# Performance work log

Measured on AMD Instinct MI355X. Metric: run time of the kernel, lower is better.

## Reference

```python
import jax, jax.numpy as jnp
import numpy as np

N, F_IN, HID, EMB, HEADS, E = 20000, 256, 256, 128, 8, 160000
NEG_SLOPE = 0.2


def setup_inputs() -> dict:
    key = jax.random.key(0)
    ks = jax.random.split(key, 16)
    s = lambda fan: 1.0 / np.sqrt(fan)
    inp = {
        "x": jax.random.normal(ks[0], (N, F_IN), jnp.float32),
        "edge_index": jax.random.randint(ks[1], (2, E), 0, N, jnp.int64),
        "W1": jax.random.normal(ks[2], (F_IN, HID), jnp.float32) * s(F_IN),
        "b1": jnp.zeros((HID,), jnp.float32),
        "W2": jax.random.normal(ks[3], (HID, HID), jnp.float32) * s(HID),
        "b2": jnp.zeros((HID,), jnp.float32),
        "W3": jax.random.normal(ks[4], (HID, EMB), jnp.float32) * s(HID),
        "b3": jnp.zeros((EMB,), jnp.float32),
        "Wg": jax.random.normal(ks[5], (EMB, HEADS * EMB), jnp.float32) * s(EMB),
        "att_src": jax.random.normal(ks[6], (HEADS, EMB), jnp.float32) * s(EMB),
        "att_dst": jax.random.normal(ks[7], (HEADS, EMB), jnp.float32) * s(EMB),
        "bg": jnp.zeros((HEADS * EMB,), jnp.float32),
        "Wh1": jax.random.normal(ks[8], (HEADS * EMB, HID), jnp.float32) * s(HEADS * EMB),
        "bh1": jnp.zeros((HID,), jnp.float32),
        "Wh2": jax.random.normal(ks[9], (HID, 1), jnp.float32) * s(HID),
        "bh2": jnp.zeros((1,), jnp.float32),
    }
    return inp


def _gcn(x, W, b, src, dst, dinv):
    h = x @ W                                   # [N, out]
    msg = h[src] * (dinv[src] * dinv[dst])[:, None]  # gather + edge scale
    return jax.ops.segment_sum(msg, dst, N) + b


def _gat(x, Wg, att_src, att_dst, bg, src, dst):
    h = (x @ Wg).reshape(N, HEADS, EMB)          # [N, H, C]
    a_s = jnp.einsum('nhc,hc->nh', h, att_src)   # [N, H]
    a_d = jnp.einsum('nhc,hc->nh', h, att_dst)
    e = jax.nn.leaky_relu(a_s[src] + a_d[dst], NEG_SLOPE)  # [Etot, H]
    m = jax.ops.segment_max(e, dst, N)           # per-dst softmax max
    ex = jnp.exp(e - m[dst])
    denom = jax.ops.segment_sum(ex, dst, N)
    alpha = ex / denom[dst]                      # [Etot, H]
    out = jax.ops.segment_sum(h[src] * alpha[:, :, None], dst, N)
    return out.reshape(N, HEADS * EMB) + bg


def reference(x, edge_index, W1, b1, W2, b2, W3, b3, Wg, att_src, att_dst, bg, Wh1, bh1, Wh2, bh2):
    loops = jnp.arange(N, dtype=edge_index.dtype)
    src = jnp.concatenate([edge_index[0], loops])
    dst = jnp.concatenate([edge_index[1], loops])
    deg = jax.ops.segment_sum(jnp.ones_like(dst, dtype=x.dtype), dst, N)
    dinv = jax.lax.rsqrt(jnp.maximum(deg, 1.0))  # deg >= 1 due to self-loops

    h = jax.nn.relu(_gcn(x, W1, b1, src, dst, dinv))
    h = jax.nn.relu(_gcn(h, W2, b2, src, dst, dinv))
    h = jax.nn.relu(_gcn(h, W3, b3, src, dst, dinv))
    h = _gat(h, Wg, att_src, att_dst, bg, src, dst)
    z = jax.nn.relu(h @ Wh1 + bh1)
    logits = (z @ Wh2 + bh2).squeeze(-1)         # [N]
    w = jax.nn.sigmoid(logits)
    return jax.nn.softmax(w, axis=0)
```

## Files before the change

kernel.cpp:

```cpp
#include <hip/hip_runtime.h>
#include <math.h>

#define NN 20000
#define HEADS 8
#define GDIM 1024
#define M_PAD 20096

typedef _Float16 f16;
typedef f16 f16x2  __attribute__((ext_vector_type(2)));
typedef f16 f16x4v __attribute__((ext_vector_type(4)));
typedef f16 f16x8v __attribute__((ext_vector_type(8)));
typedef float f32x4 __attribute__((ext_vector_type(4)));

__device__ __forceinline__ float lrelu(float x){ return x > 0.f ? x : 0.2f*x; }

__global__ __launch_bounds__(256) void init_k(int* __restrict__ zbase, int zn,
        const float* __restrict__ W1, const float* __restrict__ W2, const float* __restrict__ W3,
        const float* __restrict__ Wg, const float* __restrict__ Wh1,
        f16* __restrict__ wt1, f16* __restrict__ wt2, f16* __restrict__ wt3,
        f16* __restrict__ wtg, f16* __restrict__ wth1)
{
    int t = blockIdx.x*256 + threadIdx.x;
    if (t < zn){ zbase[t] = 0; return; }
    t -= zn;
    if (t < 65536){ int k = t >> 8, n = t & 255; wt1[n*256 + k] = (f16)W1[t]; return; }
    t -= 65536;
    if (t < 65536){ int k = t >> 8, n = t & 255; wt2[n*256 + k] = (f16)W2[t]; return; }
    t -= 65536;
    if (t < 32768){ int k = t >> 7, n = t & 127; wt3[n*256 + k] = (f16)W3[t]; return; }
    t -= 32768;
    if (t < 131072){ int k = t >> 10, n = t & 1023; wtg[n*128 + k] = (f16)Wg[t]; return; }
    t -= 131072;
    if (t < 262144){ int k = t >> 8, n = t & 255; wth1[n*1024 + k] = (f16)Wh1[t]; return; }
}

__global__ __launch_bounds__(256) void hist_k(const int* __restrict__ dst, int* __restrict__ cnt, int E){
    int i = blockIdx.x*256 + threadIdx.x;
    if (i < E) atomicAdd(&cnt[dst[i]], 1);
}
__global__ __launch_bounds__(1024) void scan_k(const int* __restrict__ cnt, int* __restrict__ row_off,
                                               float* __restrict__ dinv){
    __shared__ int tot[1024];
    int t = threadIdx.x;
    const int CH = 20;
    int base = t*CH;
    int loc[CH]; int s = 0;
    #pragma unroll
    for (int i = 0; i < CH; ++i){
        int v = (base+i < NN) ? cnt[base+i] : 0;
        loc[i] = s; s += v;
    }
    tot[t] = s; __syncthreads();
    for (int off = 1; off < 1024; off <<= 1){
        int v = (t >= off) ? tot[t-off] : 0;
        __syncthreads();
        tot[t] += v;
        __syncthreads();
    }
    int pre = (t == 0) ? 0 : tot[t-1];
    #pragma unroll
    for (int i = 0; i < CH; ++i)
        if (base+i < NN){
            row_off[base+i] = pre + loc[i];
            dinv[base+i] = rsqrtf((float)cnt[base+i] + 1.f);
        }
    if (t == 1023) row_off[NN] = tot[1023];
}
__global__ __launch_bounds__(256) void scatter_k(const int* __restrict__ src, const int* __restrict__ dst,
        const int* __restrict__ row_off, int* __restrict__ cursor, int* __restrict__ src_sorted, int E){
    int i = blockIdx.x*256 + threadIdx.x;
    if (i >= E) return;
    int d = dst[i];
    int pos = row_off[d] + atomicAdd(&cursor[d], 1);
    src_sorted[pos] = src[i];
}

template<int EPI, int BN, bool A_F32, bool RELU, bool HAS_BIAS>
__global__ __launch_bounds__(256,2) void gemm_f16_k(
        const void* __restrict__ Av, const f16* __restrict__ Bt,
        const float* __restrict__ bias, void* __restrict__ C,
        const float* __restrict__ att_s, const float* __restrict__ att_d,
        float* __restrict__ as_out, float* __restrict__ ad_out,
        const float* __restrict__ Wh2, float* __restrict__ logit,
        int M, int N, int K)
{
    constexpr int WN = BN/2;
    constexpr int NJ = WN/16;
    __shared__ __align__(16) f16 As[128*32];
    __shared__ __align__(16) f16 Bs[BN*32];
    __shared__ float sred[2][128][2];
    const int tid  = threadIdx.x;
    const int lane = tid & 63;
    const int wave = tid >> 6;
    const int wm = (wave >> 1) * 64, wn = (wave & 1) * WN;
    const int l15 = lane & 15, quad = lane >> 4;
    const int m0 = blockIdx.y * 128, n0 = blockIdx.x * BN;

    const int r1 = tid >> 2;
    const int ce = (tid & 3) * 8;
    const int rowA0 = m0 + r1, rowA1 = rowA0 + 64;
    const f16*  Ah = (const f16*)Av;
    const float* Af = (const float*)Av;
    const f16* B0 = Bt + (size_t)(n0 + r1) * K + ce;
    const f16* B1 = B0 + (size_t)64 * K;

    f32x4 acc[4][NJ] = {};
    for (int k0 = 0; k0 < K; k0 += 32){
        if (A_F32){
            f16x8v h0 = {}, h1 = {};
            if (rowA0 < M){
                float4 p = *(const float4*)(Af + (size_t)rowA0*K + k0 + ce);
                float4 q = *(const float4*)(Af + (size_t)rowA0*K + k0 + ce + 4);
                h0[0]=(f16)p.x; h0[1]=(f16)p.y; h0[2]=(f16)p.z; h0[3]=(f16)p.w;
                h0[4]=(f16)q.x; h0[5]=(f16)q.y; h0[6]=(f16)q.z; h0[7]=(f16)q.w;
            }
            if (rowA1 < M){
                float4 p = *(const float4*)(Af + (size_t)rowA1*K + k0 + ce);
                float4 q = *(const float4*)(Af + (size_t)rowA1*K + k0 + ce + 4);
                h1[0]=(f16)p.x; h1[1]=(f16)p.y; h1[2]=(f16)p.z; h1[3]=(f16)p.w;
                h1[4]=(f16)q.x; h1[5]=(f16)q.y; h1[6]=(f16)q.z; h1[7]=(f16)q.w;
            }
            *(f16x8v*)&As[tid*8]        = h0;
            *(f16x8v*)&As[tid*8 + 2048] = h1;
        } else {
            *(uint4*)&As[tid*8]        = *(const uint4*)(Ah + (size_t)rowA0*K + k0 + ce);
            *(uint4*)&As[tid*8 + 2048] = *(const uint4*)(Ah + (size_t)rowA1*K + k0 + ce);
        }
        *(uint4*)&Bs[tid*8] = *(const uint4*)(B0 + k0);
        if (BN == 128)
            *(uint4*)&Bs[tid*8 + 2048] = *(const uint4*)(B1 + k0);
        __syncthreads();
        f16x8v af[4], bf[NJ];
        #pragma unroll
        for (int i = 0; i < 4; ++i)
            af[i] = *(const f16x8v*)&As[(wm + i*16 + l15)*32 + quad*8];
        #pragma unroll
        for (int j = 0; j < NJ; ++j)
            bf[j] = *(const f16x8v*)&Bs[(wn + j*16 + l15)*32 + quad*8];
        #pragma unroll
        for (int i = 0; i < 4; ++i)
            #pragma unroll
            for (int j = 0; j < NJ; ++j)
                acc[i][j] = __builtin_amdgcn_mfma_f32_16x16x32_f16(af[i], bf[j], acc[i][j], 0, 0, 0);
        __syncthreads();
    }

    if (EPI == 2){
        float b4[NJ], w4[NJ];
        #pragma unroll
        for (int j = 0; j < NJ; ++j){
            int cg = n0 + wn + j*16 + l15;
            b4[j] = bias[cg]; w4[j] = Wh2[cg];
        }
        #pragma unroll
        for (int i = 0; i < 4; ++i)
            #pragma unroll
            for (int r = 0; r < 4; ++r){
                float ps = 0.f;
                #pragma unroll
                for (int j = 0; j < NJ; ++j){
                    float v = fmaxf(acc[i][j][r] + b4[j], 0.f);
                    ps = fmaf(v, w4[j], ps);
                }
                ps += __shfl_xor(ps, 1, 64); ps += __shfl_xor(ps, 2, 64);
                ps += __shfl_xor(ps, 4, 64); ps += __shfl_xor(ps, 8, 64);
                if (l15 == 0){
                    int row = m0 + wm + i*16 + quad*4 + r;
                    if (row < M) unsafeAtomicAdd(&logit[row], ps);
                }
            }
        return;
    }

    #pragma unroll
    for (int i = 0; i < 4; ++i){
        int rb = m0 + wm + i*16 + quad*4;
        #pragma unroll
        for (int j = 0; j < NJ; ++j){
            int col = n0 + wn + j*16 + l15;
            float bv = HAS_BIAS ? bias[col] : 0.f;
            #pragma unroll
            for (int r = 0; r < 4; ++r){
                int row = rb + r;
                if (row >= M) continue;
                float v = acc[i][j][r] + bv;
                if (RELU) v = fmaxf(v, 0.f);
                ((f16*)C)[(size_t)row*N + col] = (f16)v;
            }
        }
    }

    if (EPI == 1){
        const int h = blockIdx.x;
        float ats[NJ], atd[NJ];
        #pragma unroll
        for (int j = 0; j < NJ; ++j){
            int c = wn + j*16 + l15;
            ats[j] = att_s[h*128 + c]; atd[j] = att_d[h*128 + c];
        }
        #pragma unroll
        for (int i = 0; i < 4; ++i)
            #pragma unroll
            for (int r = 0; r < 4; ++r){
                float ps = 0.f, pd = 0.f;
                #pragma unroll
                for (int j = 0; j < NJ; ++j){
                    float a = acc[i][j][r];
                    ps = fmaf(a, ats[j], ps); pd = fmaf(a, atd[j], pd);
                }
                ps += __shfl_xor(ps, 1, 64); ps += __shfl_xor(ps, 2, 64);
                ps += __shfl_xor(ps, 4, 64); ps += __shfl_xor(ps, 8, 64);
                pd += __shfl_xor(pd, 1, 64); pd += __shfl_xor(pd, 2, 64);
                pd += __shfl_xor(pd, 4, 64); pd += __shfl_xor(pd, 8, 64);
                if (l15 == 0){
                    int rl = wm + i*16 + quad*4 + r;
                    sred[0][rl][wn >> 6] = ps;
                    sred[1][rl][wn >> 6] = pd;
                }
            }
        __syncthreads();
        if (tid < 128){
            int row = m0 + tid;
            if (row < M){
                as_out[row*HEADS + h] = sred[0][tid][0] + sred[0][tid][1];
                ad_out[row*HEADS + h] = sred[1][tid][0] + sred[1][tid][1];
            }
        }
    }
}

template<int F>
__global__ __launch_bounds__(256) void gcn_agg_f16_k(const f16* __restrict__ h, const int* __restrict__ row_off,
        const int* __restrict__ srcs, const float* __restrict__ dinv, const float* __restrict__ bias,
        f16* __restrict__ out)
{
    int wv = (blockIdx.x*256 + threadIdx.x) >> 6;
    int lane = threadIdx.x & 63;
    if (wv >= NN) return;
    float di = dinv[wv];
    int p = row_off[wv], r1 = row_off[wv+1];
    if (F == 256){
        f16x4v v = *(const f16x4v*)(h + (size_t)wv*256 + lane*4);
        float c = di*di;
        float a0 = (float)v[0]*c, a1 = (float)v[1]*c, a2 = (float)v[2]*c, a3 = (float)v[3]*c;
        for (; p+4 <= r1; p += 4){
            int s0 = srcs[p], s1 = srcs[p+1], s2 = srcs[p+2], s3 = srcs[p+3];
            float c0 = dinv[s0]*di, c1 = dinv[s1]*di, c2 = dinv[s2]*di, c3 = dinv[s3]*di;
            f16x4v u0 = *(const f16x4v*)(h + (size_t)s0*256 + lane*4);
            f16x4v u1 = *(const f16x4v*)(h + (size_t)s1*256 + lane*4);
            f16x4v u2 = *(const f16x4v*)(h + (size_t)s2*256 + lane*4);
            f16x4v u3 = *(const f16x4v*)(h + (size_t)s3*256 + lane*4);
            a0 = fmaf((float)u3[0], c3, fmaf((float)u2[0], c2, fmaf((float)u1[0], c1, fmaf((float)u0[0], c0, a0))));
            a1 = fmaf((float)u3[1], c3, fmaf((float)u2[1], c2, fmaf((float)u1[1], c1, fmaf((float)u0[1], c0, a1))));
            a2 = fmaf((float)u3[2], c3, fmaf((float)u2[2], c2, fmaf((float)u1[2], c1, fmaf((float)u0[2], c0, a2))));
            a3 = fmaf((float)u3[3], c3, fmaf((float)u2[3], c2, fmaf((float)u1[3], c1, fmaf((float)u0[3], c0, a3))));
        }
        for (; p < r1; ++p){
            int s0 = srcs[p];
            float c0 = dinv[s0]*di;
            f16x4v u0 = *(const f16x4v*)(h + (size_t)s0*256 + lane*4);
            a0 = fmaf((float)u0[0], c0, a0); a1 = fmaf((float)u0[1], c0, a1);
            a2 = fmaf((float)u0[2], c0, a2); a3 = fmaf((float)u0[3], c0, a3);
        }
        float4 bv = *(const float4*)(bias + lane*4);
        f16x4v o;
        o[0] = (f16)fmaxf(a0 + bv.x, 0.f); o[1] = (f16)fmaxf(a1 + bv.y, 0.f);
        o[2] = (f16)fmaxf(a2 + bv.z, 0.f); o[3] = (f16)fmaxf(a3 + bv.w, 0.f);
        *(f16x4v*)(out + (size_t)wv*256 + lane*4) = o;
    } else {
        f16x2 v = *(const f16x2*)(h + (size_t)wv*128 + lane*2);
        float c = di*di;
        float a0 = (float)v[0]*c, a1 = (float)v[1]*c;
        for (; p+4 <= r1; p += 4){
            int s0 = srcs[p], s1 = srcs[p+1], s2 = srcs[p+2], s3 = srcs[p+3];
            float c0 = dinv[s0]*di, c1 = dinv[s1]*di, c2 = dinv[s2]*di, c3 = dinv[s3]*di;
            f16x2 u0 = *(const f16x2*)(h + (size_t)s0*128 + lane*2);
            f16x2 u1 = *(const f16x2*)(h + (size_t)s1*128 + lane*2);
            f16x2 u2 = *(const f16x2*)(h + (size_t)s2*128 + lane*2);
            f16x2 u3 = *(const f16x2*)(h + (size_t)s3*128 + lane*2);
            a0 = fmaf((float)u3[0], c3, fmaf((float)u2[0], c2, fmaf((float)u1[0], c1, fmaf((float)u0[0], c0, a0))));
            a1 = fmaf((float)u3[1], c3, fmaf((float)u2[1], c2, fmaf((float)u1[1], c1, fmaf((float)u0[1], c0, a1))));
        }
        for (; p < r1; ++p){
            int s0 = srcs[p];
            float c0 = dinv[s0]*di;
            f16x2 u0 = *(const f16x2*)(h + (size_t)s0*128 + lane*2);
            a0 = fmaf((float)u0[0], c0, a0); a1 = fmaf((float)u0[1], c0, a1);
        }
        float2 bv = *(const float2*)(bias + lane*2);
        f16x2 o;
        o[0] = (f16)fmaxf(a0 + bv.x, 0.f); o[1] = (f16)fmaxf(a1 + bv.y, 0.f);
        *(f16x2*)(out + (size_t)wv*128 + lane*2) = o;
    }
}

__global__ __launch_bounds__(256) void gat_soft_k(const int* __restrict__ row_off, const int* __restrict__ srcs,
        const float* __restrict__ a_s, const float* __restrict__ a_d,
        float* __restrict__ ex_sorted, float* __restrict__ alpha_self, float* __restrict__ inv_den)
{
    int t = blockIdx.x*256 + threadIdx.x;
    if (t >= NN*HEADS) return;
    int d = t >> 3, h = t & 7;
    float ad = a_d[t];
    float eself = lrelu(a_s[t] + ad);
    float m = eself;
    int r0 = row_off[d], r1 = row_off[d+1];
    for (int p = r0; p < r1; ++p){
        int s = srcs[p];
        m = fmaxf(m, lrelu(a_s[s*HEADS + h] + ad));
    }
    float den = expf(eself - m);
    for (int p = r0; p < r1; ++p){
        int s = srcs[p];
        float x = expf(lrelu(a_s[s*HEADS + h] + ad) - m);
        ex_sorted[(size_t)p*HEADS + h] = x;
        den += x;
    }
    float id = 1.f / den;
    alpha_self[t] = expf(eself - m) * id;
    inv_den[t]    = id;
}
__global__ __launch_bounds__(256) void gat_out_f16_k(const f16* __restrict__ hg, const int* __restrict__ row_off,
        const int* __restrict__ srcs, const float* __restrict__ exs, const float* __restrict__ aself,
        const float* __restrict__ idn, const float* __restrict__ bg, f16* __restrict__ gat)
{
    int gw = (blockIdx.x*256 + threadIdx.x) >> 6;
    int lane = threadIdx.x & 63;
    int node = gw >> 1;
    if (node >= NN) return;
    int colbase = (gw & 1)*512 + lane*8;
    int hh = colbase >> 7;
    int nh = node*HEADS + hh;
    float as = aself[nh];
    float id = idn[nh];
    const f16* table = hg + colbase;
    f16x8v v = *(const f16x8v*)(table + (size_t)node*GDIM);
    float acc[8];
    #pragma unroll
    for (int q = 0; q < 8; ++q) acc[q] = (float)v[q]*as;
    int p = row_off[node], r1 = row_off[node+1];
    for (; p+4 <= r1; p += 4){
        int s0 = srcs[p], s1 = srcs[p+1], s2 = srcs[p+2], s3 = srcs[p+3];
        float al0 = exs[(size_t)p*HEADS + hh] * id;
        float al1 = exs[(size_t)(p+1)*HEADS + hh] * id;
        float al2 = exs[(size_t)(p+2)*HEADS + hh] * id;
        float al3 = exs[(size_t)(p+3)*HEADS + hh] * id;
        f16x8v u0 = *(const f16x8v*)(table + (size_t)s0*GDIM);
        f16x8v u1 = *(const f16x8v*)(table + (size_t)s1*GDIM);
        f16x8v u2 = *(const f16x8v*)(table + (size_t)s2*GDIM);
        f16x8v u3 = *(const f16x8v*)(table + (size_t)s3*GDIM);
        #pragma unroll
        for (int q = 0; q < 8; ++q)
            acc[q] = fmaf((float)u3[q], al3, fmaf((float)u2[q], al2,
                     fmaf((float)u1[q], al1, fmaf((float)u0[q], al0, acc[q]))));
    }
    for (; p < r1; ++p){
        int s0 = srcs[p];
        float al0 = exs[(size_t)p*HEADS + hh] * id;
        f16x8v u0 = *(const f16x8v*)(table + (size_t)s0*GDIM);
        #pragma unroll
        for (int q = 0; q < 8; ++q) acc[q] = fmaf((float)u0[q], al0, acc[q]);
    }
    float4 b0 = *(const float4*)(bg + colbase);
    float4 b1 = *(const float4*)(bg + colbase + 4);
    f16x8v o;
    o[0]=(f16)(acc[0]+b0.x); o[1]=(f16)(acc[1]+b0.y); o[2]=(f16)(acc[2]+b0.z); o[3]=(f16)(acc[3]+b0.w);
    o[4]=(f16)(acc[4]+b1.x); o[5]=(f16)(acc[5]+b1.y); o[6]=(f16)(acc[6]+b1.z); o[7]=(f16)(acc[7]+b1.w);
    *(f16x8v*)(gat + (size_t)node*GDIM + colbase) = o;
}

__global__ __launch_bounds__(256) void head_sum_k(const float* __restrict__ logit, const float* __restrict__ bh2,
                                                  float* __restrict__ w, float* __restrict__ red){
    __shared__ float sm[256];
    int i = blockIdx.x*256 + threadIdx.x;
    float v = 0.f;
    if (i < NN){
        float s = 1.f / (1.f + expf(-(logit[i] + bh2[0])));
        w[i] = s;
        v = expf(s);
    }
    sm[threadIdx.x] = v; __syncthreads();
    for (int off = 128; off; off >>= 1){
        if (threadIdx.x < off) sm[threadIdx.x] += sm[threadIdx.x+off];
        __syncthreads();
    }
    if (!threadIdx.x) unsafeAtomicAdd(&red[0], sm[0]);
}
__global__ __launch_bounds__(256) void final_k(const float* __restrict__ w, const float* __restrict__ red,
                                               float* __restrict__ out){
    int i = blockIdx.x*256 + threadIdx.x;
    if (i >= NN) return;
    out[i] = expf(w[i]) / red[0];
}

extern "C" void kernel_launch(void* const* d_in, const int* in_sizes, int n_in,
                              void* d_out, int out_size, void* d_ws, size_t ws_size,
                              hipStream_t stream) {
    const float* x   = (const float*)d_in[0];
    const int*   ei  = (const int*)  d_in[1];
    const float* W1  = (const float*)d_in[2];
    const float* b1  = (const float*)d_in[3];
    const float* W2  = (const float*)d_in[4];
    const float* b2  = (const float*)d_in[5];
    const float* W3  = (const float*)d_in[6];
    const float* b3  = (const float*)d_in[7];
    const float* Wg  = (const float*)d_in[8];
    const float* att_src = (const float*)d_in[9];
    const float* att_dst = (const float*)d_in[10];
    const float* bg  = (const float*)d_in[11];
    const float* Wh1 = (const float*)d_in[12];
    const float* bh1 = (const float*)d_in[13];
    const float* Wh2 = (const float*)d_in[14];
    const float* bh2 = (const float*)d_in[15];
    float* out = (float*)d_out;

    const int E = in_sizes[1] / 2;
    const int* src = ei;
    const int* dst = ei + E;

    float* ws = (float*)d_ws;
    size_t o = 0;
    auto alloc = [&](size_t nfloats){ float* p = ws + o; o += (nfloats + 3) & ~(size_t)3; return p; };
    int* cnt    = (int*)alloc(NN);
    int* cursor = (int*)alloc(NN);
    float* logit= alloc(NN);
    float* red  = alloc(8);
    const int ZERO_N = 3*NN + 8;

    f16* wt1   = (f16*)alloc(65536/2);
    f16* wt2   = (f16*)alloc(65536/2);
    f16* wt3   = (f16*)alloc(32768/2);
    f16* wtg   = (f16*)alloc(131072/2);
    f16* wth1  = (f16*)alloc(262144/2);
    f16* fH    = (f16*)alloc((size_t)M_PAD*256/2);
    f16* fG    = (f16*)alloc((size_t)M_PAD*256/2);
    f16* hg    = (f16*)alloc((size_t)M_PAD*GDIM/2);
    f16* gat   = (f16*)alloc((size_t)M_PAD*GDIM/2);
    float* dinv = alloc(NN);
    float* a_s  = alloc((size_t)NN*HEADS);
    float* a_d  = alloc((size_t)NN*HEADS);
    float* aself= alloc((size_t)NN*HEADS);
    float* idn  = alloc((size_t)NN*HEADS);
    float* exs  = alloc((size_t)E*HEADS);
    float* wsig = alloc(NN);
    int* row_off= (int*)alloc(NN+1);
    int* src_srt= (int*)alloc(E);

    const int nb  = (NN + 255)/256;
    const int eb  = (E + 255)/256;
    const int nwb = (NN + 3)/4;
    const dim3 blk(256);
    const int MT = M_PAD/128;

    const int INIT_T = ZERO_N + 65536*2 + 32768 + 131072 + 262144;
    init_k<<<(INIT_T + 255)/256, blk, 0, stream>>>(cnt, ZERO_N, W1, W2, W3, Wg, Wh1,
                                                   wt1, wt2, wt3, wtg, wth1);
    hist_k<<<eb, blk, 0, stream>>>(dst, cnt, E);
    scan_k<<<1, 1024, 0, stream>>>(cnt, row_off, dinv);
    scatter_k<<<eb, blk, 0, stream>>>(src, dst, row_off, cursor, src_srt, E);

    gemm_f16_k<0,64,true,false,false><<<dim3(4, MT), blk, 0, stream>>>(
        x, wt1, nullptr, fH, nullptr, nullptr, nullptr, nullptr, nullptr, nullptr, NN, 256, 256);
    gcn_agg_f16_k<256><<<nwb, blk, 0, stream>>>(fH, row_off, src_srt, dinv, b1, fG);
    gemm_f16_k<0,64,false,false,false><<<dim3(4, MT), blk, 0, stream>>>(
        fG, wt2, nullptr, fH, nullptr, nullptr, nullptr, nullptr, nullptr, nullptr, NN, 256, 256);
    gcn_agg_f16_k<256><<<nwb, blk, 0, stream>>>(fH, row_off, src_srt, dinv, b2, fG);
    gemm_f16_k<0,64,false,false,false><<<dim3(2, MT), blk, 0, stream>>>(
        fG, wt3, nullptr, fH, nullptr, nullptr, nullptr, nullptr, nullptr, nullptr, NN, 128, 256);
    gcn_agg_f16_k<128><<<nwb, blk, 0, stream>>>(fH, row_off, src_srt, dinv, b3, fG);

    gemm_f16_k<1,128,false,false,false><<<dim3(8, MT), blk, 0, stream>>>(
        fG, wtg, nullptr, hg, att_src, att_dst, a_s, a_d, nullptr, nullptr, NN, 1024, 128);
    gat_soft_k<<<(NN*HEADS)/256, blk, 0, stream>>>(row_off, src_srt, a_s, a_d, exs, aself, idn);
    gat_out_f16_k<<<NN/2, blk, 0, stream>>>(hg, row_off, src_srt, exs, aself, idn, bg, gat);

    gemm_f16_k<2,128,false,true,true><<<dim3(2, MT), blk, 0, stream>>>(
        gat, wth1, bh1, nullptr, nullptr, nullptr, nullptr, nullptr, Wh2, logit, NN, 256, 1024);

    head_sum_k<<<nb, blk, 0, stream>>>(logit, bh2, wsig, red);
    final_k<<<nb, blk, 0, stream>>>(wsig, red, out);
}
```

Baseline: 379.6 us.

## Fold GAT projection into attention vectors and head weight, aggregate raw embeddings

Removes the 128→1024 GAT projection GEMM. Attention logits are computed directly from the 128-dim embeddings using precomputed Wg·att vectors. The weighted neighbour aggregation now runs on the 128-dim input, once per head, and the resulting 1024-wide aggregate is multiplied by a fused Wg·Wh1 weight with a folded bias. This avoids writing and gathering the 1024-wide hg table. The cost is a new per-call weight-fusion kernel, and fp16 rounding now applies to the fused weight product instead.

```diff
diff --git a/kernel.cpp b/kernel.cpp
--- a/kernel.cpp
+++ b/kernel.cpp
@@ -3,7 +3,6 @@
 
 #define NN 20000
 #define HEADS 8
-#define GDIM 1024
 #define M_PAD 20096
 
 typedef _Float16 f16;
@@ -16,9 +15,9 @@
 
 __global__ __launch_bounds__(256) void init_k(int* __restrict__ zbase, int zn,
         const float* __restrict__ W1, const float* __restrict__ W2, const float* __restrict__ W3,
-        const float* __restrict__ Wg, const float* __restrict__ Wh1,
+        const float* __restrict__ Wg, const float* __restrict__ att_src, const float* __restrict__ att_dst,
         f16* __restrict__ wt1, f16* __restrict__ wt2, f16* __restrict__ wt3,
-        f16* __restrict__ wtg, f16* __restrict__ wth1)
+        float* __restrict__ was_s, float* __restrict__ was_d)
 {
     int t = blockIdx.x*256 + threadIdx.x;
     if (t < zn){ zbase[t] = 0; return; }
@@ -29,9 +28,53 @@
     t -= 65536;
     if (t < 32768){ int k = t >> 7, n = t & 127; wt3[n*256 + k] = (f16)W3[t]; return; }
     t -= 32768;
-    if (t < 131072){ int k = t >> 10, n = t & 1023; wtg[n*128 + k] = (f16)Wg[t]; return; }
-    t -= 131072;
-    if (t < 262144){ int k = t >> 8, n = t & 255; wth1[n*1024 + k] = (f16)Wh1[t]; return; }
+    if (t < 2048){
+        int which = t >> 10, r = t & 1023, k = r >> 3, h = r & 7;
+        const float* att = which ? att_dst : att_src;
+        float s = 0.f;
+        for (int c = 0; c < 128; ++c)
+            s = fmaf(Wg[k*1024 + h*128 + c], att[h*128 + c], s);
+        (which ? was_d : was_s)[k*8 + h] = s;
+    }
+}
+
+__global__ __launch_bounds__(256) void wc_k(const float* __restrict__ Wg, const float* __restrict__ Wh1,
+        const float* __restrict__ bg, const float* __restrict__ bh1,
+        f16* __restrict__ wc_t, float* __restrict__ biasc)
+{
+    __shared__ float col[1024];
+    __shared__ float red[256];
+    const int j = blockIdx.x, t = threadIdx.x;
+    float bsum = 0.f;
+    #pragma unroll
+    for (int i = 0; i < 4; ++i){
+        int kk = i*256 + t;
+        float v = Wh1[(size_t)kk*256 + j];
+        col[kk] = v;
+        bsum = fmaf(bg[kk], v, bsum);
+    }
+    red[t] = bsum; __syncthreads();
+    for (int off = 128; off; off >>= 1){
+        if (t < off) red[t] += red[t+off];
+        __syncthreads();
+    }
+    if (!t) biasc[j] = red[0] + bh1[j];
+    #pragma unroll
+    for (int i = 0; i < 4; ++i){
+        int k = i*256 + t;
+        int h = k >> 7, kk = k & 127;
+        const float* wg = Wg + (size_t)kk*1024 + h*128;
+        const float* cl = col + h*128;
+        float s = 0.f;
+        for (int c = 0; c < 128; c += 4){
+            float4 wv = *(const float4*)(wg + c);
+            s = fmaf(wv.x, cl[c],   s);
+            s = fmaf(wv.y, cl[c+1], s);
+            s = fmaf(wv.z, cl[c+2], s);
+            s = fmaf(wv.w, cl[c+3], s);
+        }
+        wc_t[(size_t)j*1024 + k] = (f16)s;
+    }
 }
 
 __global__ __launch_bounds__(256) void hist_k(const int* __restrict__ dst, int* __restrict__ cnt, int E){
@@ -79,8 +122,6 @@
 __global__ __launch_bounds__(256,2) void gemm_f16_k(
         const void* __restrict__ Av, const f16* __restrict__ Bt,
         const float* __restrict__ bias, void* __restrict__ C,
-        const float* __restrict__ att_s, const float* __restrict__ att_d,
-        float* __restrict__ as_out, float* __restrict__ ad_out,
         const float* __restrict__ Wh2, float* __restrict__ logit,
         int M, int N, int K)
 {
@@ -88,7 +129,6 @@
     constexpr int NJ = WN/16;
     __shared__ __align__(16) f16 As[128*32];
     __shared__ __align__(16) f16 Bs[BN*32];
-    __shared__ float sred[2][128][2];
     const int tid  = threadIdx.x;
     const int lane = tid & 63;
     const int wave = tid >> 6;
@@ -189,44 +229,6 @@
             }
         }
     }
-
-    if (EPI == 1){
-        const int h = blockIdx.x;
-        float ats[NJ], atd[NJ];
-        #pragma unroll
-        for (int j = 0; j < NJ; ++j){
-            int c = wn + j*16 + l15;
-            ats[j] = att_s[h*128 + c]; atd[j] = att_d[h*128 + c];
-        }
-        #pragma unroll
-        for (int i = 0; i < 4; ++i)
-            #pragma unroll
-            for (int r = 0; r < 4; ++r){
-                float ps = 0.f, pd = 0.f;
-                #pragma unroll
-                for (int j = 0; j < NJ; ++j){
-                    float a = acc[i][j][r];
-                    ps = fmaf(a, ats[j], ps); pd = fmaf(a, atd[j], pd);
-                }
-                ps += __shfl_xor(ps, 1, 64); ps += __shfl_xor(ps, 2, 64);
-                ps += __shfl_xor(ps, 4, 64); ps += __shfl_xor(ps, 8, 64);
-                pd += __shfl_xor(pd, 1, 64); pd += __shfl_xor(pd, 2, 64);
-                pd += __shfl_xor(pd, 4, 64); pd += __shfl_xor(pd, 8, 64);
-                if (l15 == 0){
-                    int rl = wm + i*16 + quad*4 + r;
-                    sred[0][rl][wn >> 6] = ps;
-                    sred[1][rl][wn >> 6] = pd;
-                }
-            }
-        __syncthreads();
-        if (tid < 128){
-            int row = m0 + tid;
-            if (row < M){
-                as_out[row*HEADS + h] = sred[0][tid][0] + sred[0][tid][1];
-                ad_out[row*HEADS + h] = sred[1][tid][0] + sred[1][tid][1];
-            }
-        }
-    }
 }
 
 template<int F>
@@ -294,6 +296,30 @@
     }
 }
 
+__global__ __launch_bounds__(256) void asd_k(const f16* __restrict__ fG,
+        const float* __restrict__ was_s, const float* __restrict__ was_d,
+        float* __restrict__ a_s, float* __restrict__ a_d)
+{
+    int wv = (blockIdx.x*256 + threadIdx.x) >> 6;
+    int lane = threadIdx.x & 63;
+    if (wv >= NN) return;
+    f16x2 v = *(const f16x2*)(fG + (size_t)wv*128 + lane*2);
+    float v0 = (float)v[0], v1 = (float)v[1];
+    const float* ws = was_s + lane*16;
+    const float* wd = was_d + lane*16;
+    #pragma unroll
+    for (int h = 0; h < 8; ++h){
+        float s = fmaf(v1, ws[8+h], v0*ws[h]);
+        float d = fmaf(v1, wd[8+h], v0*wd[h]);
+        #pragma unroll
+        for (int off = 1; off < 64; off <<= 1){
+            s += __shfl_xor(s, off, 64);
+            d += __shfl_xor(d, off, 64);
+        }
+        if (lane == 0){ a_s[wv*8 + h] = s; a_d[wv*8 + h] = d; }
+    }
+}
+
 __global__ __launch_bounds__(256) void gat_soft_k(const int* __restrict__ row_off, const int* __restrict__ srcs,
         const float* __restrict__ a_s, const float* __restrict__ a_d,
         float* __restrict__ ex_sorted, float* __restrict__ alpha_self, float* __restrict__ inv_den)
@@ -320,53 +346,61 @@
     alpha_self[t] = expf(eself - m) * id;
     inv_den[t]    = id;
 }
-__global__ __launch_bounds__(256) void gat_out_f16_k(const f16* __restrict__ hg, const int* __restrict__ row_off,
+
+__global__ __launch_bounds__(256) void agg_k(const f16* __restrict__ fG, const int* __restrict__ row_off,
         const int* __restrict__ srcs, const float* __restrict__ exs, const float* __restrict__ aself,
-        const float* __restrict__ idn, const float* __restrict__ bg, f16* __restrict__ gat)
-{
-    int gw = (blockIdx.x*256 + threadIdx.x) >> 6;
+        const float* __restrict__ idn, f16* __restrict__ agg)
+{
+    int wv = (blockIdx.x*256 + threadIdx.x) >> 6;
     int lane = threadIdx.x & 63;
-    int node = gw >> 1;
-    if (node >= NN) return;
-    int colbase = (gw & 1)*512 + lane*8;
-    int hh = colbase >> 7;
-    int nh = node*HEADS + hh;
-    float as = aself[nh];
-    float id = idn[nh];
-    const f16* table = hg + colbase;
-    f16x8v v = *(const f16x8v*)(table + (size_t)node*GDIM);
-    float acc[8];
-    #pragma unroll
-    for (int q = 0; q < 8; ++q) acc[q] = (float)v[q]*as;
-    int p = row_off[node], r1 = row_off[node+1];
-    for (; p+4 <= r1; p += 4){
-        int s0 = srcs[p], s1 = srcs[p+1], s2 = srcs[p+2], s3 = srcs[p+3];
-        float al0 = exs[(size_t)p*HEADS + hh] * id;
-        float al1 = exs[(size_t)(p+1)*HEADS + hh] * id;
-        float al2 = exs[(size_t)(p+2)*HEADS + hh] * id;
-        float al3 = exs[(size_t)(p+3)*HEADS + hh] * id;
-        f16x8v u0 = *(const f16x8v*)(table + (size_t)s0*GDIM);
-        f16x8v u1 = *(const f16x8v*)(table + (size_t)s1*GDIM);
-        f16x8v u2 = *(const f16x8v*)(table + (size_t)s2*GDIM);
-        f16x8v u3 = *(const f16x8v*)(table + (size_t)s3*GDIM);
-        #pragma unroll
-        for (int q = 0; q < 8; ++q)
-            acc[q] = fmaf((float)u3[q], al3, fmaf((float)u2[q], al2,
-                     fmaf((float)u1[q], al1, fmaf((float)u0[q], al0, acc[q]))));
+    if (wv >= NN) return;
+    f16x2 v = *(const f16x2*)(fG + (size_t)wv*128 + lane*2);
+    float v0 = (float)v[0], v1 = (float)v[1];
+    float id[8], acc0[8], acc1[8];
+    #pragma unroll
+    for (int h = 0; h < 8; ++h){
+        float as = aself[wv*8 + h];
+        acc0[h] = v0*as; acc1[h] = v1*as;
+        id[h] = idn[wv*8 + h];
+    }
+    int p = row_off[wv], r1 = row_off[wv+1];
+    for (; p+2 <= r1; p += 2){
+        int s0 = srcs[p], s1 = srcs[p+1];
+        f16x2 u0 = *(const f16x2*)(fG + (size_t)s0*128 + lane*2);
+        f16x2 u1 = *(const f16x2*)(fG + (size_t)s1*128 + lane*2);
+        float4 ea = *(const float4*)(exs + (size_t)p*8);
+        float4 eb = *(const float4*)(exs + (size_t)p*8 + 4);
+        float4 fa = *(const float4*)(exs + (size_t)(p+1)*8);
+        float4 fb = *(const float4*)(exs + (size_t)(p+1)*8 + 4);
+        float u00=(float)u0[0], u01=(float)u0[1], u10=(float)u1[0], u11=(float)u1[1];
+        float e0[8] = {ea.x,ea.y,ea.z,ea.w,eb.x,eb.y,eb.z,eb.w};
+        float e1[8] = {fa.x,fa.y,fa.z,fa.w,fb.x,fb.y,fb.z,fb.w};
+        #pragma unroll
+        for (int h = 0; h < 8; ++h){
+            float al0 = e0[h]*id[h], al1 = e1[h]*id[h];
+            acc0[h] = fmaf(u10, al1, fmaf(u00, al0, acc0[h]));
+            acc1[h] = fmaf(u11, al1, fmaf(u01, al0, acc1[h]));
+        }
     }
     for (; p < r1; ++p){
         int s0 = srcs[p];
-        float al0 = exs[(size_t)p*HEADS + hh] * id;
-        f16x8v u0 = *(const f16x8v*)(table + (size_t)s0*GDIM);
-        #pragma unroll
-        for (int q = 0; q < 8; ++q) acc[q] = fmaf((float)u0[q], al0, acc[q]);
-    }
-    float4 b0 = *(const float4*)(bg + colbase);
-    float4 b1 = *(const float4*)(bg + colbase + 4);
-    f16x8v o;
-    o[0]=(f16)(acc[0]+b0.x); o[1]=(f16)(acc[1]+b0.y); o[2]=(f16)(acc[2]+b0.z); o[3]=(f16)(acc[3]+b0.w);
-    o[4]=(f16)(acc[4]+b1.x); o[5]=(f16)(acc[5]+b1.y); o[6]=(f16)(acc[6]+b1.z); o[7]=(f16)(acc[7]+b1.w);
-    *(f16x8v*)(gat + (size_t)node*GDIM + colbase) = o;
+        f16x2 u0 = *(const f16x2*)(fG + (size_t)s0*128 + lane*2);
+        float4 ea = *(const float4*)(exs + (size_t)p*8);
+        float4 eb = *(const float4*)(exs + (size_t)p*8 + 4);
+        float u00=(float)u0[0], u01=(float)u0[1];
+        float e0[8] = {ea.x,ea.y,ea.z,ea.w,eb.x,eb.y,eb.z,eb.w};
+        #pragma unroll
+        for (int h = 0; h < 8; ++h){
+            float al0 = e0[h]*id[h];
+            acc0[h] = fmaf(u00, al0, acc0[h]);
+            acc1[h] = fmaf(u01, al0, acc1[h]);
+        }
+    }
+    #pragma unroll
+    for (int h = 0; h < 8; ++h){
+        f16x2 o; o[0] = (f16)acc0[h]; o[1] = (f16)acc1[h];
+        *(f16x2*)(agg + (size_t)wv*1024 + h*128 + lane*2) = o;
+    }
 }
 
 __global__ __launch_bounds__(256) void head_sum_k(const float* __restrict__ logit, const float* __restrict__ bh2,
@@ -430,12 +464,13 @@
     f16* wt1   = (f16*)alloc(65536/2);
     f16* wt2   = (f16*)alloc(65536/2);
     f16* wt3   = (f16*)alloc(32768/2);
-    f16* wtg   = (f16*)alloc(131072/2);
-    f16* wth1  = (f16*)alloc(262144/2);
+    f16* wc_t  = (f16*)alloc(262144/2);
+    float* was_s = alloc(1024);
+    float* was_d = alloc(1024);
+    float* biasc = alloc(256);
     f16* fH    = (f16*)alloc((size_t)M_PAD*256/2);
     f16* fG    = (f16*)alloc((size_t)M_PAD*256/2);
-    f16* hg    = (f16*)alloc((size_t)M_PAD*GDIM/2);
-    f16* gat   = (f16*)alloc((size_t)M_PAD*GDIM/2);
+    f16* agg   = (f16*)alloc((size_t)M_PAD*1024/2);
     float* dinv = alloc(NN);
     float* a_s  = alloc((size_t)NN*HEADS);
     float* a_d  = alloc((size_t)NN*HEADS);
@@ -452,30 +487,30 @@
     const dim3 blk(256);
     const int MT = M_PAD/128;
 
-    const int INIT_T = ZERO_N + 65536*2 + 32768 + 131072 + 262144;
-    init_k<<<(INIT_T + 255)/256, blk, 0, stream>>>(cnt, ZERO_N, W1, W2, W3, Wg, Wh1,
-                                                   wt1, wt2, wt3, wtg, wth1);
+    const int INIT_T = ZERO_N + 65536*2 + 32768 + 2048;
+    init_k<<<(INIT_T + 255)/256, blk, 0, stream>>>(cnt, ZERO_N, W1, W2, W3, Wg, att_src, att_dst,
+                                                   wt1, wt2, wt3, was_s, was_d);
+    wc_k<<<256, blk, 0, stream>>>(Wg, Wh1, bg, bh1, wc_t, biasc);
     hist_k<<<eb, blk, 0, stream>>>(dst, cnt, E);
     scan_k<<<1, 1024, 0, stream>>>(cnt, row_off, dinv);
     scatter_k<<<eb, blk, 0, stream>>>(src, dst, row_off, cursor, src_srt, E);
 
     gemm_f16_k<0,64,true,false,false><<<dim3(4, MT), blk, 0, stream>>>(
-        x, wt1, nullptr, fH, nullptr, nullptr, nullptr, nullptr, nullptr, nullptr, NN, 256, 256);
+        x, wt1, nullptr, fH, nullptr, nullptr, NN, 256, 256);
     gcn_agg_f16_k<256><<<nwb, blk, 0, stream>>>(fH, row_off, src_srt, dinv, b1, fG);
     gemm_f16_k<0,64,false,false,false><<<dim3(4, MT), blk, 0, stream>>>(
-        fG, wt2, nullptr, fH, nullptr, nullptr, nullptr, nullptr, nullptr, nullptr, NN, 256, 256);
+        fG, wt2, nullptr, fH, nullptr, nullptr, NN, 256, 256);
     gcn_agg_f16_k<256><<<nwb, blk, 0, stream>>>(fH, row_off, src_srt, dinv, b2, fG);
     gemm_f16_k<0,64,false,false,false><<<dim3(2, MT), blk, 0, stream>>>(
-        fG, wt3, nullptr, fH, nullptr, nullptr, nullptr, nullptr, nullptr, nullptr, NN, 128, 256);
+        fG, wt3, nullptr, fH, nullptr, nullptr, NN, 128, 256);
     gcn_agg_f16_k<128><<<nwb, blk, 0, stream>>>(fH, row_off, src_srt, dinv, b3, fG);
 
-    gemm_f16_k<1,128,false,false,false><<<dim3(8, MT), blk, 0, stream>>>(
-        fG, wtg, nullptr, hg, att_src, att_dst, a_s, a_d, nullptr, nullptr, NN, 1024, 128);
+    asd_k<<<nwb, blk, 0, stream>>>(fG, was_s, was_d, a_s, a_d);
     gat_soft_k<<<(NN*HEADS)/256, blk, 0, stream>>>(row_off, src_srt, a_s, a_d, exs, aself, idn);
-    gat_out_f16_k<<<NN/2, blk, 0, stream>>>(hg, row_off, src_srt, exs, aself, idn, bg, gat);
+    agg_k<<<nwb, blk, 0, stream>>>(fG, row_off, src_srt, exs, aself, idn, agg);
 
     gemm_f16_k<2,128,false,true,true><<<dim3(2, MT), blk, 0, stream>>>(
-        gat, wth1, bh1, nullptr, nullptr, nullptr, nullptr, nullptr, Wh2, logit, NN, 256, 1024);
+        agg, wc_t, biasc, nullptr, Wh2, logit, NN, 256, 1024);
 
     head_sum_k<<<nb, blk, 0, stream>>>(logit, bh2, wsig, red);
     final_k<<<nb, blk, 0, stream>>>(wsig, red, out);
```

New measurement: 414.5 us. 1.09x slower.
